# Kernel optimization log

Hardware: AMD Instinct MI355X
Metric: run time of the kernel (lower is better)

Reference implementation:

```python
import jax, jax.numpy as jnp
import numpy as np
import math

B, N, D = 8, 2048, 64


def setup_inputs() -> dict:
    key = jax.random.key(0)
    kq, kk, kv, kd = jax.random.split(key, 4)
    Q = jax.random.normal(kq, (B, N, D), dtype=jnp.float32)
    K = jax.random.normal(kk, (B, N, D), dtype=jnp.float32)
    V = jax.random.normal(kv, (B, N, D), dtype=jnp.float32)
    dist_matrix = jax.random.uniform(kd, (N, N), dtype=jnp.float32)
    return {"Q": Q, "K": K, "V": V, "dist_matrix": dist_matrix}


def rescale_distance_matrix(dist_matrix):
    # (1 + e^1) / (1 + exp(1 - dist))
    c = 1.0
    return (c + math.e) / (c + jnp.exp(c - dist_matrix))


def reference(Q, K, V, dist_matrix):
    d_k = K.shape[-1]
    inv_sqrt_dk = 1.0 / math.sqrt(d_k)
    # [B, N, N] raw attention logits
    qk = jnp.einsum("bnd,bmd->bnm", Q, K)
    # ReLU then multiply by rescaled distance matrix [N, N] on the right
    scores = jnp.matmul(jax.nn.relu(qk), rescale_distance_matrix(dist_matrix)) * inv_sqrt_dk
    attn = jax.nn.softmax(scores, axis=-1)
    context = jnp.einsum("bnm,bmd->bnd", attn, V)
    return context
```

## Files before the change

kernel.cpp:

```cpp
#include <hip/hip_runtime.h>


typedef _Float16 f16;
typedef _Float16 f16x8 __attribute__((ext_vector_type(8)));
typedef float    f32x4 __attribute__((ext_vector_type(4)));

#define AS1C(p) ((const __attribute__((address_space(1))) void*)(p))
#define AS3(p)  ((__attribute__((address_space(3))) void*)(p))

__device__ __forceinline__ f16x8 cvt_f16x8(float4 a, float4 b){
  f16x8 v;
  v[0]=(f16)a.x; v[1]=(f16)a.y; v[2]=(f16)a.z; v[3]=(f16)a.w;
  v[4]=(f16)b.x; v[5]=(f16)b.y; v[6]=(f16)b.z; v[7]=(f16)b.w;
  return v;
}

__launch_bounds__(256, 2)
__global__ void k_qk(const float* __restrict__ Q, const float* __restrict__ Km,
                     const float* __restrict__ V, const float* __restrict__ Dm,
                     f16* __restrict__ Ph, f16* __restrict__ RhT,
                     f16* __restrict__ VhT){
  __shared__ char shm[36864];
  const int bid = blockIdx.x;
  const int t = threadIdx.x;

  if (bid >= 2048){
    f16* tl = (f16*)shm;
    const int c = t & 63, g = t >> 6;
    if (bid < 3072){
      const int pid = bid - 2048;
      const int k0 = (pid & 31)*64, m0 = (pid >> 5)*64;
#pragma unroll
      for (int i=0;i<16;++i){
        int k = g*16 + i;
        float d = Dm[(size_t)(k0 + k)*2048 + m0 + c];
        tl[k*65 + c] = (f16)(3.7182818284590452f / (1.0f + __expf(1.0f - d)));
      }
      __syncthreads();
#pragma unroll
      for (int i=0;i<16;++i){
        int m = g*16 + i;
        RhT[(size_t)(m0 + m)*2048 + k0 + c] = tl[c*65 + m];
      }
    } else {
      const int pid = bid - 3072;
      const int m0 = (pid & 31)*64, b = pid >> 5;
#pragma unroll
      for (int i=0;i<16;++i){
        int m = g*16 + i;
        tl[m*65 + c] = (f16)V[((size_t)b*2048 + m0 + m)*64 + c];
      }
      __syncthreads();
#pragma unroll
      for (int i=0;i<16;++i){
        int d = g*16 + i;
        VhT[((size_t)b*64 + d)*2048 + m0 + c] = tl[c*65 + d];
      }
    }
    return;
  }

  f16* Qt = (f16*)shm;
  f16* Kt = (f16*)(shm + 18432);
  f16* Tt = (f16*)shm;

  const int w = t>>6, l = t&63, lr = l&15, q = l>>4;
  const int m0 = (bid & 15)*128, n0 = ((bid>>4) & 15)*128, b = bid >> 8;
  const int wr = (w>>1)*64, wc = (w&1)*64;
  const float* Qb = Q  + ((size_t)b*2048 + n0)*64;
  const float* Kb = Km + ((size_t)b*2048 + m0)*64;

  const int sr = t>>3, sc = t&7;
#pragma unroll
  for (int j=0;j<4;++j){
    int row = sr + 32*j;
    const float* p  = Qb + (size_t)row*64 + sc*8;
    *(f16x8*)(Qt + row*72 + sc*8) = cvt_f16x8(*(const float4*)p, *(const float4*)(p+4));
    const float* pk = Kb + (size_t)row*64 + sc*8;
    *(f16x8*)(Kt + row*72 + sc*8) = cvt_f16x8(*(const float4*)pk, *(const float4*)(pk+4));
  }
  __syncthreads();

  f32x4 acc[4][4] = {};
#pragma unroll
  for (int kc=0;kc<2;++kc){
    f16x8 af[4], bf[4];
#pragma unroll
    for (int ti=0;ti<4;++ti) af[ti] = *(const f16x8*)(Qt + (wr+16*ti+lr)*72 + kc*32 + q*8);
#pragma unroll
    for (int tj=0;tj<4;++tj) bf[tj] = *(const f16x8*)(Kt + (wc+16*tj+lr)*72 + kc*32 + q*8);
#pragma unroll
    for (int ti=0;ti<4;++ti)
#pragma unroll
      for (int tj=0;tj<4;++tj)
        acc[ti][tj] = __builtin_amdgcn_mfma_f32_16x16x32_f16(af[ti], bf[tj], acc[ti][tj], 0,0,0);
  }
  __syncthreads();
#pragma unroll
  for (int ti=0;ti<4;++ti)
#pragma unroll
    for (int tj=0;tj<4;++tj)
#pragma unroll
      for (int r=0;r<4;++r)
        Tt[(wr+16*ti+4*q+r)*136 + wc+16*tj+lr] = (f16)(fmaxf(acc[ti][tj][r],0.f)*0.125f);
  __syncthreads();
  const int g16 = t&15, r0 = t>>4;
#pragma unroll
  for (int j=0;j<8;++j){
    int row = r0 + 16*j;
    *(f16x8*)(Ph + ((size_t)b*2048 + n0 + row)*2048 + m0 + g16*8) =
        *(const f16x8*)(Tt + row*136 + g16*8);
  }
}

__launch_bounds__(256, 2)
__global__ void k_attn(const f16* __restrict__ Ph, const f16* __restrict__ RhT,
                       const f16* __restrict__ VhT, f16* __restrict__ Op,
                       float* __restrict__ mp, float* __restrict__ lp){
  __shared__ char smem[49152];
  f16*  Pbuf = (f16*)smem;
  f16*  Rbuf = (f16*)(smem + 16384);
  f16*  El   = (f16*)smem;
  float* stat_max = (float*)(smem + 33792);
  float* stat_sum = (float*)(smem + 34816);

  const int t = threadIdx.x, w = t>>6, l = t&63, lr = l&15, q = l>>4;
  const int bid = blockIdx.x;
  const int jq = bid & 7, nbb = bid >> 3, b = nbb & 7, nb = nbb >> 3;
  const int n0 = nb*128, jg = jq*256;
  const int wc = w*64;

  const f16* Pblk = Ph  + ((size_t)b*2048 + n0)*2048;
  const f16* Vb   = VhT + (size_t)b*64*2048;

  const f16* srcP[2];
  const f16* srcR[4];
#pragma unroll
  for (int i=0;i<2;++i){
    int slot = i*256 + t, row = slot>>2, g = slot&3;
    srcP[i] = Pblk + (size_t)row*2048 + (g ^ ((row>>1)&3))*8;
  }
#pragma unroll
  for (int i=0;i<4;++i){
    int slot = i*256 + t, row = slot>>2, g = slot&3;
    srcR[i] = RhT + (size_t)(jg + row)*2048 + (g ^ ((row>>1)&3))*8;
  }

  auto stage = [&](int kc){
    const int cb = kc & 1, k0 = kc*32;
#pragma unroll
    for (int i=0;i<2;++i)
      __builtin_amdgcn_global_load_lds(AS1C(srcP[i] + k0),
                                       AS3(Pbuf + cb*4096 + i*2048 + w*512), 16, 0, 0);
#pragma unroll
    for (int i=0;i<4;++i)
      __builtin_amdgcn_global_load_lds(AS1C(srcR[i] + k0),
                                       AS3(Rbuf + cb*8192 + i*2048 + w*512), 16, 0, 0);
  };

  const int swz = (lr>>1)&3;
  f32x4 acc[8][4] = {};
  f32x4 Oacc[2][2][2] = {};

  stage(0);
#pragma unroll 2
  for (int kc = 0; kc < 64; ++kc){
    __syncthreads();
    if (kc < 63) stage(kc+1);
    const int cb = kc & 1;
    const f16* Pb = Pbuf + cb*4096;
    const f16* Rb = Rbuf + cb*8192;
    f16x8 bf[4];
#pragma unroll
    for (int tj=0;tj<4;++tj)
      bf[tj] = *(const f16x8*)(Rb + (wc + 16*tj + lr)*32 + (q ^ swz)*8);
#pragma unroll
    for (int ti=0;ti<8;++ti){
      f16x8 af = *(const f16x8*)(Pb + (16*ti + lr)*32 + (q ^ swz)*8);
#pragma unroll
      for (int tj=0;tj<4;++tj)
        acc[ti][tj] = __builtin_amdgcn_mfma_f32_16x16x32_f16(af, bf[tj], acc[ti][tj], 0,0,0);
    }
  }
  __syncthreads();

#pragma unroll
  for (int p=0;p<2;++p){
    float pm[4][4];
#pragma unroll
    for (int ti=0;ti<4;++ti)
#pragma unroll
      for (int r=0;r<4;++r)
        pm[ti][r] = fmaxf(fmaxf(acc[4*p+ti][0][r], acc[4*p+ti][1][r]),
                          fmaxf(acc[4*p+ti][2][r], acc[4*p+ti][3][r]));
#pragma unroll
    for (int mm=1;mm<16;mm<<=1)
#pragma unroll
      for (int ti=0;ti<4;++ti)
#pragma unroll
        for (int r=0;r<4;++r)
          pm[ti][r] = fmaxf(pm[ti][r], __shfl_xor(pm[ti][r], mm));
    if (lr == 0)
#pragma unroll
      for (int ti=0;ti<4;++ti)
#pragma unroll
        for (int r=0;r<4;++r)
          stat_max[(16*ti + 4*q + r)*4 + w] = pm[ti][r];
    __syncthreads();

    float Mn[4][4], ps[4][4];
#pragma unroll
    for (int ti=0;ti<4;++ti)
#pragma unroll
      for (int r=0;r<4;++r){
        int row = 16*ti + 4*q + r;
        float4 s4 = *(const float4*)&stat_max[row*4];
        Mn[ti][r] = fmaxf(fmaxf(s4.x,s4.y), fmaxf(s4.z,s4.w));
        ps[ti][r] = 0.f;
      }
#pragma unroll
    for (int ti=0;ti<4;++ti)
#pragma unroll
      for (int tj=0;tj<4;++tj)
#pragma unroll
        for (int r=0;r<4;++r){
          float e = __expf(acc[4*p+ti][tj][r] - Mn[ti][r]);
          ps[ti][r] += e;
          El[(16*ti + 4*q + r)*264 + wc + 16*tj + lr] = (f16)e;
        }
#pragma unroll
    for (int mm=1;mm<16;mm<<=1)
#pragma unroll
      for (int ti=0;ti<4;++ti)
#pragma unroll
        for (int r=0;r<4;++r)
          ps[ti][r] += __shfl_xor(ps[ti][r], mm);
    if (lr == 0)
#pragma unroll
      for (int ti=0;ti<4;++ti)
#pragma unroll
        for (int r=0;r<4;++r)
          stat_sum[(16*ti + 4*q + r)*4 + w] = ps[ti][r];
    __syncthreads();

    if (w == 0 && lr == 0)
#pragma unroll
      for (int ti=0;ti<4;++ti)
#pragma unroll
        for (int r=0;r<4;++r){
          int row = 16*ti + 4*q + r;
          float4 s4 = *(const float4*)&stat_sum[row*4];
          mp[bid*128 + 64*p + row] = Mn[ti][r];
          lp[bid*128 + 64*p + row] = s4.x + s4.y + s4.z + s4.w;
        }

    const int erb = 32*(w&1), vcb = 32*(w>>1);
#pragma unroll
    for (int ks=0; ks<8; ++ks){
      f16x8 ae[2], bv[2];
#pragma unroll
      for (int a=0;a<2;++a)
        ae[a] = *(const f16x8*)(El + (erb + 16*a + lr)*264 + ks*32 + q*8);
#pragma unroll
      for (int bb=0;bb<2;++bb)
        bv[bb] = *(const f16x8*)(Vb + (size_t)(vcb + 16*bb + lr)*2048 + jg + ks*32 + q*8);
#pragma unroll
      for (int a=0;a<2;++a)
#pragma unroll
        for (int bb=0;bb<2;++bb)
          Oacc[p][a][bb] = __builtin_amdgcn_mfma_f32_16x16x32_f16(ae[a], bv[bb], Oacc[p][a][bb], 0,0,0);
    }
    __syncthreads();
  }

#pragma unroll
  for (int p=0;p<2;++p)
#pragma unroll
    for (int a=0;a<2;++a)
#pragma unroll
      for (int bb=0;bb<2;++bb)
#pragma unroll
        for (int r=0;r<4;++r){
          int row = 64*p + 32*(w&1) + 16*a + 4*q + r;
          int col = 32*(w>>1) + 16*bb + lr;
          Op[((size_t)bid*128 + row)*64 + col] = (f16)Oacc[p][a][bb][r];
        }
}

__global__ void k_comb(const f16* __restrict__ Op, const float* __restrict__ mp,
                       const float* __restrict__ lp, float* __restrict__ out){
  const int rb = blockIdx.x;
  const int b = rb & 7, nb = rb >> 3;
  const int bid0 = rb << 3;
  const int t = threadIdx.x;
  const int row = t >> 1, half = t & 1;

  float m_[8], a_[8];
  float M = -1e30f, den = 0.f;
#pragma unroll
  for (int i=0;i<8;++i){ m_[i] = mp[(bid0+i)*128 + row]; M = fmaxf(M, m_[i]); }
#pragma unroll
  for (int i=0;i<8;++i){ a_[i] = __expf(m_[i] - M); den += a_[i]*lp[(bid0+i)*128 + row]; }
  float inv = 1.0f / den;

#pragma unroll
  for (int g=0;g<4;++g){
    int c0 = half*32 + g*8;
    float o[8] = {};
#pragma unroll
    for (int i=0;i<8;++i){
      f16x8 v = *(const f16x8*)(Op + ((size_t)(bid0+i)*128 + row)*64 + c0);
#pragma unroll
      for (int e=0;e<8;++e) o[e] += a_[i]*(float)v[e];
    }
    float4 o0, o1;
    o0.x=o[0]*inv; o0.y=o[1]*inv; o0.z=o[2]*inv; o0.w=o[3]*inv;
    o1.x=o[4]*inv; o1.y=o[5]*inv; o1.z=o[6]*inv; o1.w=o[7]*inv;
    float* dst = out + ((size_t)b*2048 + nb*128 + row)*64 + c0;
    *(float4*)dst = o0;
    *(float4*)(dst+4) = o1;
  }
}

extern "C" void kernel_launch(void* const* d_in, const int* in_sizes, int n_in,
                              void* d_out, int out_size, void* d_ws, size_t ws_size,
                              hipStream_t stream){
  (void)in_sizes; (void)n_in; (void)out_size; (void)ws_size;
  const float* Q  = (const float*)d_in[0];
  const float* K  = (const float*)d_in[1];
  const float* V  = (const float*)d_in[2];
  const float* Dm = (const float*)d_in[3];
  float* out = (float*)d_out;
  char* ws = (char*)d_ws;
  f16* Ph  = (f16*)ws;
  f16* RhT = (f16*)(ws + (size_t)64*1024*1024);
  f16* VhT = (f16*)(ws + (size_t)72*1024*1024);
  f16* Op  = (f16*)(ws + (size_t)74*1024*1024);
  float* mpp = (float*)(ws + (size_t)90*1024*1024);
  float* lpp = mpp + 1024*128;

  k_qk   <<<dim3(3328), 256, 0, stream>>>(Q, K, V, Dm, Ph, RhT, VhT);
  k_attn <<<dim3(1024), 256, 0, stream>>>(Ph, RhT, VhT, Op, mpp, lpp);
  k_comb <<<dim3(128),  256, 0, stream>>>(Op, mpp, lpp, out);
}
```

Measured before the change: 248.3 us.

## Triple-buffer attn GEMM loads, raise qk occupancy, widen combine grid

The P·R GEMM in k_attn moves from double to triple buffering, with explicit vmcnt waits, raw barriers and setprio around the MFMA block, so loads run two stages ahead of compute. Shared memory grows to 72KB, which could limit k_attn blocks per CU. k_qk's launch bounds go from 2 to 3 waves per SIMD, which may cap its registers. k_comb is split into 4x more blocks, one 8-column chunk per thread, to improve parallelism in the final reduction.

Measured after the change: 252.7 us. About the same (+1.8%).

```diff
diff --git a/kernel.cpp b/kernel.cpp
--- a/kernel.cpp
+++ b/kernel.cpp
@@ -15,7 +15,7 @@
   return v;
 }
 
-__launch_bounds__(256, 2)
+__launch_bounds__(256, 3)
 __global__ void k_qk(const float* __restrict__ Q, const float* __restrict__ Km,
                      const float* __restrict__ V, const float* __restrict__ Dm,
                      f16* __restrict__ Ph, f16* __restrict__ RhT,
@@ -117,9 +117,9 @@
 __global__ void k_attn(const f16* __restrict__ Ph, const f16* __restrict__ RhT,
                        const f16* __restrict__ VhT, f16* __restrict__ Op,
                        float* __restrict__ mp, float* __restrict__ lp){
-  __shared__ char smem[49152];
+  __shared__ char smem[73728];
   f16*  Pbuf = (f16*)smem;
-  f16*  Rbuf = (f16*)(smem + 16384);
+  f16*  Rbuf = (f16*)(smem + 24576);
   f16*  El   = (f16*)smem;
   float* stat_max = (float*)(smem + 33792);
   float* stat_sum = (float*)(smem + 34816);
@@ -146,34 +146,30 @@
     srcR[i] = RhT + (size_t)(jg + row)*2048 + (g ^ ((row>>1)&3))*8;
   }
 
-  auto stage = [&](int kc){
-    const int cb = kc & 1, k0 = kc*32;
+  auto stage = [&](int kc, int sb){
+    const int k0 = kc*32;
 #pragma unroll
     for (int i=0;i<2;++i)
       __builtin_amdgcn_global_load_lds(AS1C(srcP[i] + k0),
-                                       AS3(Pbuf + cb*4096 + i*2048 + w*512), 16, 0, 0);
+                                       AS3(Pbuf + sb*4096 + i*2048 + w*512), 16, 0, 0);
 #pragma unroll
     for (int i=0;i<4;++i)
       __builtin_amdgcn_global_load_lds(AS1C(srcR[i] + k0),
-                                       AS3(Rbuf + cb*8192 + i*2048 + w*512), 16, 0, 0);
+                                       AS3(Rbuf + sb*8192 + i*2048 + w*512), 16, 0, 0);
   };
 
   const int swz = (lr>>1)&3;
   f32x4 acc[8][4] = {};
   f32x4 Oacc[2][2][2] = {};
 
-  stage(0);
-#pragma unroll 2
-  for (int kc = 0; kc < 64; ++kc){
-    __syncthreads();
-    if (kc < 63) stage(kc+1);
-    const int cb = kc & 1;
+  auto compute = [&](int cb){
     const f16* Pb = Pbuf + cb*4096;
     const f16* Rb = Rbuf + cb*8192;
     f16x8 bf[4];
 #pragma unroll
     for (int tj=0;tj<4;++tj)
       bf[tj] = *(const f16x8*)(Rb + (wc + 16*tj + lr)*32 + (q ^ swz)*8);
+    __builtin_amdgcn_s_setprio(1);
 #pragma unroll
     for (int ti=0;ti<8;++ti){
       f16x8 af = *(const f16x8*)(Pb + (16*ti + lr)*32 + (q ^ swz)*8);
@@ -181,7 +177,31 @@
       for (int tj=0;tj<4;++tj)
         acc[ti][tj] = __builtin_amdgcn_mfma_f32_16x16x32_f16(af, bf[tj], acc[ti][tj], 0,0,0);
     }
-  }
+    __builtin_amdgcn_s_setprio(0);
+  };
+
+  stage(0, 0);
+  stage(1, 1);
+  int cur = 0;
+  for (int kc = 0; kc < 62; ++kc){
+    asm volatile("s_waitcnt vmcnt(6)" ::: "memory");
+    __builtin_amdgcn_s_barrier();
+    __builtin_amdgcn_sched_barrier(0);
+    int sb = cur + 2; if (sb >= 3) sb -= 3;
+    stage(kc + 2, sb);
+    compute(cur);
+    cur += 1; if (cur >= 3) cur -= 3;
+  }
+  asm volatile("s_waitcnt vmcnt(6)" ::: "memory");
+  __builtin_amdgcn_s_barrier();
+  __builtin_amdgcn_sched_barrier(0);
+  compute(cur);
+  cur += 1; if (cur >= 3) cur -= 3;
+  asm volatile("s_waitcnt vmcnt(0)" ::: "memory");
+  __builtin_amdgcn_s_barrier();
+  __builtin_amdgcn_sched_barrier(0);
+  compute(cur);
+
   __syncthreads();
 
 #pragma unroll
@@ -289,11 +309,13 @@
 
 __global__ void k_comb(const f16* __restrict__ Op, const float* __restrict__ mp,
                        const float* __restrict__ lp, float* __restrict__ out){
-  const int rb = blockIdx.x;
+  const int rb = blockIdx.x >> 2;
+  const int qr = blockIdx.x & 3;
   const int b = rb & 7, nb = rb >> 3;
   const int bid0 = rb << 3;
   const int t = threadIdx.x;
-  const int row = t >> 1, half = t & 1;
+  const int row = qr*32 + (t >> 3);
+  const int c0 = (t & 7)*8;
 
   float m_[8], a_[8];
   float M = -1e30f, den = 0.f;
@@ -303,23 +325,19 @@
   for (int i=0;i<8;++i){ a_[i] = __expf(m_[i] - M); den += a_[i]*lp[(bid0+i)*128 + row]; }
   float inv = 1.0f / den;
 
-#pragma unroll
-  for (int g=0;g<4;++g){
-    int c0 = half*32 + g*8;
-    float o[8] = {};
-#pragma unroll
-    for (int i=0;i<8;++i){
-      f16x8 v = *(const f16x8*)(Op + ((size_t)(bid0+i)*128 + row)*64 + c0);
-#pragma unroll
-      for (int e=0;e<8;++e) o[e] += a_[i]*(float)v[e];
-    }
-    float4 o0, o1;
-    o0.x=o[0]*inv; o0.y=o[1]*inv; o0.z=o[2]*inv; o0.w=o[3]*inv;
-    o1.x=o[4]*inv; o1.y=o[5]*inv; o1.z=o[6]*inv; o1.w=o[7]*inv;
-    float* dst = out + ((size_t)b*2048 + nb*128 + row)*64 + c0;
-    *(float4*)dst = o0;
-    *(float4*)(dst+4) = o1;
-  }
+  float o[8] = {};
+#pragma unroll
+  for (int i=0;i<8;++i){
+    f16x8 v = *(const f16x8*)(Op + ((size_t)(bid0+i)*128 + row)*64 + c0);
+#pragma unroll
+    for (int e=0;e<8;++e) o[e] += a_[i]*(float)v[e];
+  }
+  float4 o0, o1;
+  o0.x=o[0]*inv; o0.y=o[1]*inv; o0.z=o[2]*inv; o0.w=o[3]*inv;
+  o1.x=o[4]*inv; o1.y=o[5]*inv; o1.z=o[6]*inv; o1.w=o[7]*inv;
+  float* dst = out + ((size_t)b*2048 + nb*128 + row)*64 + c0;
+  *(float4*)dst = o0;
+  *(float4*)(dst+4) = o1;
 }
 
 extern "C" void kernel_launch(void* const* d_in, const int* in_sizes, int n_in,
@@ -341,5 +359,5 @@
 
   k_qk   <<<dim3(3328), 256, 0, stream>>>(Q, K, V, Dm, Ph, RhT, VhT);
   k_attn <<<dim3(1024), 256, 0, stream>>>(Ph, RhT, VhT, Op, mpp, lpp);
-  k_comb <<<dim3(128),  256, 0, stream>>>(Op, mpp, lpp, out);
-}
+  k_comb <<<dim3(512),  256, 0, stream>>>(Op, mpp, lpp, out);
+}
```
